# Kernel optimization log

Measured on AMD Instinct MI355X. Metric: run time of the kernel, lower is better.

## Reference

```python
import jax, jax.numpy as jnp
import numpy as np

N = 200000
D, H, W = 32, 480, 360   # sparse voxel grid (z, y, x)
CIN, COUT = 32, 64
BN_EPS = 1e-5


def _build_sparse_structure(seed=0):
    rng = np.random.default_rng(seed)
    lin = rng.choice(D * H * W, size=N, replace=False).astype(np.int64)
    d = lin // (H * W)
    h = (lin // W) % H
    w = lin % W
    lookup = np.full(D * H * W, -1, np.int32)
    lookup[lin] = np.arange(N, dtype=np.int32)

    def build_nbr(offsets):
        out = np.full((len(offsets), N), -1, np.int32)
        for k, (dd, dh, dw) in enumerate(offsets):
            nd, nh, nw = d + dd, h + dh, w + dw
            valid = (nd >= 0) & (nd < D) & (nh >= 0) & (nh < H) & (nw >= 0) & (nw < W)
            nl = (nd * H + nh) * W + nw
            out[k, valid] = lookup[nl[valid]]
        return out

    # conv1x3: kernel (1,3,3) -> offsets over (h, w)
    offs_a = [(0, dh, dw) for dh in (-1, 0, 1) for dw in (-1, 0, 1)]
    # conv3x1: kernel (3,1,3) -> offsets over (d, w)
    offs_b = [(dd, 0, dw) for dd in (-1, 0, 1) for dw in (-1, 0, 1)]
    return build_nbr(offs_a), build_nbr(offs_b)


def setup_inputs() -> dict:
    key = jax.random.key(0)
    ks = jax.random.split(key, 6)
    nbr_a, nbr_b = _build_sparse_structure()
    s = 0.05
    return {
        "feats": jax.random.normal(ks[0], (N, CIN), jnp.float32),
        "nbr_a": jnp.asarray(nbr_a),
        "nbr_b": jnp.asarray(nbr_b),
        "W1": jax.random.normal(ks[1], (9, CIN, COUT), jnp.float32) * s,
        "W1_2": jax.random.normal(ks[2], (9, COUT, COUT), jnp.float32) * s,
        "W2": jax.random.normal(ks[3], (9, CIN, COUT), jnp.float32) * s,
        "W3": jax.random.normal(ks[4], (9, COUT, COUT), jnp.float32) * s,
        "g0": jnp.ones((COUT,), jnp.float32), "b0": jnp.zeros((COUT,), jnp.float32),
        "g0_2": jnp.ones((COUT,), jnp.float32), "b0_2": jnp.zeros((COUT,), jnp.float32),
        "g1": jnp.ones((COUT,), jnp.float32), "b1": jnp.zeros((COUT,), jnp.float32),
        "g2": jnp.ones((COUT,), jnp.float32), "b2": jnp.zeros((COUT,), jnp.float32),
    }


def _subm_conv(x, nbr, Wk):
    # Submanifold sparse conv: gather neighbors per kernel offset, GEMM, sum.
    mask = (nbr >= 0)                                  # [K, N]
    g = x[jnp.clip(nbr, 0)] * mask[..., None]          # [K, N, Cin]
    return jnp.einsum('knc,kcd->nd', g, Wk)            # [N, Cout]


def _bn(x, g, b):
    # BatchNorm1d in training mode: biased batch stats over the voxel dim.
    m = jnp.mean(x, axis=0)
    v = jnp.var(x, axis=0)
    return g * (x - m) * jax.lax.rsqrt(v + BN_EPS) + b


def reference(feats, nbr_a, nbr_b, W1, W1_2, W2, W3,
              g0, b0, g0_2, b0_2, g1, b1, g2, b2):
    lrelu = lambda x: jax.nn.leaky_relu(x, 0.01)
    # shortcut branch: conv1x3 -> act -> bn -> conv3x1 -> bn
    sc = _subm_conv(feats, nbr_a, W1)
    sc = _bn(lrelu(sc), g0, b0)
    sc = _bn(_subm_conv(sc, nbr_b, W1_2), g0_2, b0_2)
    # main branch: conv3x1 -> act -> bn -> conv1x3 -> bn
    r = _subm_conv(feats, nbr_b, W2)
    r = _bn(lrelu(r), g1, b1)
    r = _bn(_subm_conv(r, nbr_a, W3), g2, b2)
    return r + sc
```

## Files before the change

### kernel.cpp

```cpp
#include <hip/hip_runtime.h>
#include <hip/hip_bf16.h>

#define NVOX 200000
#define CO 64

typedef short short8 __attribute__((ext_vector_type(8)));
typedef float f32x4 __attribute__((ext_vector_type(4)));

static __device__ __forceinline__ short f2bf(float f) {
    __hip_bfloat16 h = __float2bfloat16(f);
    return __builtin_bit_cast(short, h);
}

template<int CIN, bool IN_F32, bool LRELU, bool BIAS, bool OUT0_BF16, bool OUT1_BF16>
__global__ __launch_bounds__(320) void conv_mfma2(
    const void* __restrict__ xin0, const void* __restrict__ xin1,
    const int*  __restrict__ nbr0, const int* __restrict__ nbr1,
    const unsigned short* __restrict__ pack0, const unsigned short* __restrict__ pack1,
    const unsigned short* __restrict__ biasB0, const unsigned short* __restrict__ biasB1,
    void* __restrict__ out0, void* __restrict__ out1,
    float* __restrict__ ssum0, float* __restrict__ ssq0,
    float* __restrict__ ssum1, float* __restrict__ ssq1)
{
    constexpr int CHN = CIN / 32;
    const int br = blockIdx.y;
    const void* xin              = br ? xin1 : xin0;
    const int* nbr               = br ? nbr1 : nbr0;
    const unsigned short* bpack  = br ? pack1 : pack0;
    const unsigned short* biasB  = br ? biasB1 : biasB0;
    void* outp                   = br ? out1 : out0;
    float* s_sum                 = br ? ssum1 : ssum0;
    float* s_sq                  = br ? ssq1 : ssq0;
    const bool OUT_BF16          = br ? OUT1_BF16 : OUT0_BF16;

    const int lane = threadIdx.x & 63;
    const int wblk = threadIdx.x >> 6;
    const int wv   = blockIdx.x * 5 + wblk;
    const int gbase = wv * 32;
    const int g = lane >> 4, r16 = lane & 15;

    int iv[2][9];
    #pragma unroll
    for (int t = 0; t < 2; ++t)
        #pragma unroll
        for (int k = 0; k < 9; ++k)
            iv[t][k] = nbr[k * NVOX + gbase + t * 16 + r16];

    f32x4 acc[2][4];
    #pragma unroll
    for (int t = 0; t < 2; ++t)
        #pragma unroll
        for (int nt = 0; nt < 4; ++nt)
            acc[t][nt] = (f32x4){0.f, 0.f, 0.f, 0.f};

    #pragma unroll 3
    for (int k = 0; k < 9; ++k) {
        short8 bf[CHN][4];
        #pragma unroll
        for (int ch = 0; ch < CHN; ++ch)
            #pragma unroll
            for (int nt = 0; nt < 4; ++nt)
                bf[ch][nt] = *reinterpret_cast<const short8*>(
                    bpack + ((((size_t)k * CHN + ch) * 4 + nt) * 64 + lane) * 8);
        #pragma unroll
        for (int t = 0; t < 2; ++t) {
            const int ivk = iv[t][k];
            const int ivt = ivk < 0 ? 0 : ivk;
            #pragma unroll
            for (int ch = 0; ch < CHN; ++ch) {
                short8 av;
                if (IN_F32) {
                    const float* ap = (const float*)xin + (size_t)ivt * CIN + ch * 32 + g * 8;
                    float4 f0 = ((const float4*)ap)[0];
                    float4 f1 = ((const float4*)ap)[1];
                    av[0] = f2bf(f0.x); av[1] = f2bf(f0.y); av[2] = f2bf(f0.z); av[3] = f2bf(f0.w);
                    av[4] = f2bf(f1.x); av[5] = f2bf(f1.y); av[6] = f2bf(f1.z); av[7] = f2bf(f1.w);
                } else {
                    av = *reinterpret_cast<const short8*>(
                        (const unsigned short*)xin + (size_t)ivt * CIN + ch * 32 + g * 8);
                }
                if (ivk < 0) { short8 z = {0,0,0,0,0,0,0,0}; av = z; }
                #pragma unroll
                for (int nt = 0; nt < 4; ++nt)
                    acc[t][nt] = __builtin_amdgcn_mfma_f32_16x16x32_bf16(av, bf[ch][nt], acc[t][nt], 0, 0, 0);
            }
        }
    }

    if (BIAS) {
        short8 bb[4];
        #pragma unroll
        for (int nt = 0; nt < 4; ++nt)
            bb[nt] = *reinterpret_cast<const short8*>(biasB + ((size_t)nt * 64 + lane) * 8);
        #pragma unroll
        for (int t = 0; t < 2; ++t) {
            unsigned vmask = 0;
            #pragma unroll
            for (int k = 0; k < 9; ++k) vmask |= (iv[t][k] >= 0 ? 1u : 0u) << k;
            short8 vf;
            #pragma unroll
            for (int i = 0; i < 8; ++i) {
                int k9 = g * 8 + i;
                vf[i] = (k9 < 9 && ((vmask >> k9) & 1u)) ? (short)0x3F80 : (short)0;
            }
            #pragma unroll
            for (int nt = 0; nt < 4; ++nt)
                acc[t][nt] = __builtin_amdgcn_mfma_f32_16x16x32_bf16(vf, bb[nt], acc[t][nt], 0, 0, 0);
        }
    }

    float ss[4] = {0,0,0,0}, sq[4] = {0,0,0,0};
    #pragma unroll
    for (int t = 0; t < 2; ++t)
        #pragma unroll
        for (int nt = 0; nt < 4; ++nt)
            #pragma unroll
            for (int rr = 0; rr < 4; ++rr) {
                float val = acc[t][nt][rr];
                if (LRELU) val = val > 0.f ? val : 0.01f * val;
                ss[nt] += val; sq[nt] += val * val;
                const size_t o = (size_t)(gbase + t * 16 + g * 4 + rr) * CO + nt * 16 + r16;
                if (OUT_BF16) ((__hip_bfloat16*)outp)[o] = __float2bfloat16(val);
                else          ((float*)outp)[o] = val;
            }

    __shared__ float lsum[5][64];
    __shared__ float lsq[5][64];
    #pragma unroll
    for (int nt = 0; nt < 4; ++nt) {
        float a = ss[nt], b = sq[nt];
        a += __shfl_xor(a, 16); a += __shfl_xor(a, 32);
        b += __shfl_xor(b, 16); b += __shfl_xor(b, 32);
        if (lane < 16) { lsum[wblk][nt * 16 + r16] = a; lsq[wblk][nt * 16 + r16] = b; }
    }
    __syncthreads();
    if (threadIdx.x < 64) {
        float a = 0.f, b = 0.f;
        #pragma unroll
        for (int w = 0; w < 5; ++w) { a += lsum[w][threadIdx.x]; b += lsq[w][threadIdx.x]; }
        atomicAdd(s_sum + threadIdx.x, a);
        atomicAdd(s_sq  + threadIdx.x, b);
    }
}

__global__ void prepack_w32(const float* __restrict__ W1, const float* __restrict__ W2,
                            unsigned short* __restrict__ P1, unsigned short* __restrict__ P2)
{
    int s = blockIdx.x / 9, k = blockIdx.x % 9, l = threadIdx.x;
    const float* W = s ? W2 : W1;
    unsigned short* P = s ? P2 : P1;
    int g = l >> 4, r16 = l & 15;
    for (int nt = 0; nt < 4; ++nt)
        for (int i = 0; i < 8; ++i) {
            int c = g * 8 + i, j = nt * 16 + r16;
            P[(((size_t)k * 4 + nt) * 64 + l) * 8 + i] =
                (unsigned short)f2bf(W[((size_t)k * 32 + c) * 64 + j]);
        }
}

__global__ void bn_fin(const float* sum0, const float* sq0, const float* g0, const float* b0, float* a0, float* c0,
                       const float* sum1, const float* sq1, const float* g1, const float* b1, float* a1, float* c1)
{
    int j = threadIdx.x;
    const float inv_n = 1.f / (float)NVOX;
    if (blockIdx.x == 0) {
        float m = sum0[j] * inv_n;
        float v = sq0[j] * inv_n - m * m;
        float a = g0[j] * rsqrtf(v + 1e-5f);
        a0[j] = a; c0[j] = b0[j] - m * a;
    } else {
        float m = sum1[j] * inv_n;
        float v = sq1[j] * inv_n - m * m;
        float a = g1[j] * rsqrtf(v + 1e-5f);
        a1[j] = a; c1[j] = b1[j] - m * a;
    }
}

__global__ void wtrans(const float* W0, const float* a0v, const float* c0v, unsigned short* P0, float* bias0,
                       const float* W1, const float* a1v, const float* c1v, unsigned short* P1, float* bias1)
{
    int s = blockIdx.x / 9, k = blockIdx.x % 9, l = threadIdx.x;
    const float* W  = s ? W1 : W0;
    const float* av = s ? a1v : a0v;
    const float* cv = s ? c1v : c0v;
    unsigned short* P = s ? P1 : P0;
    float* bias = s ? bias1 : bias0;
    int g = l >> 4, r16 = l & 15;
    for (int ch = 0; ch < 2; ++ch)
        for (int nt = 0; nt < 4; ++nt)
            for (int i = 0; i < 8; ++i) {
                int c = ch * 32 + g * 8 + i, j = nt * 16 + r16;
                P[((((size_t)k * 2 + ch) * 4 + nt) * 64 + l) * 8 + i] =
                    (unsigned short)f2bf(av[c] * W[((size_t)k * 64 + c) * 64 + j]);
            }
    float bs = 0.f;
    for (int c = 0; c < 64; ++c) bs += cv[c] * W[((size_t)k * 64 + c) * 64 + l];
    bias[k * 64 + l] = bs;
}

__global__ void wpack_bias(const float* bias0, unsigned short* B0,
                           const float* bias1, unsigned short* B1)
{
    int s = blockIdx.x, l = threadIdx.x;
    const float* bias = s ? bias1 : bias0;
    unsigned short* B = s ? B1 : B0;
    int g = l >> 4, r16 = l & 15;
    for (int nt = 0; nt < 4; ++nt)
        for (int i = 0; i < 8; ++i) {
            int k9 = g * 8 + i;
            B[((size_t)nt * 64 + l) * 8 + i] =
                k9 < 9 ? (unsigned short)f2bf(bias[k9 * 64 + nt * 16 + r16]) : (unsigned short)0;
        }
}

__global__ void final_k(float* __restrict__ out, const __hip_bfloat16* __restrict__ sc2,
                        const float* __restrict__ a2, const float* __restrict__ c2,
                        const float* __restrict__ a02, const float* __restrict__ c02)
{
    int i = blockIdx.x * blockDim.x + threadIdx.x;
    if (i >= NVOX * CO) return;
    int ch = i & 63;
    float r = out[i];
    float s = __bfloat162float(sc2[i]);
    out[i] = a2[ch] * r + c2[ch] + a02[ch] * s + c02[ch];
}

extern "C" void kernel_launch(void* const* d_in, const int* in_sizes, int n_in,
                              void* d_out, int out_size, void* d_ws, size_t ws_size,
                              hipStream_t stream)
{
    const float* feats = (const float*)d_in[0];
    const int*   nbr_a = (const int*)d_in[1];
    const int*   nbr_b = (const int*)d_in[2];
    const float* W1    = (const float*)d_in[3];
    const float* W1_2  = (const float*)d_in[4];
    const float* W2    = (const float*)d_in[5];
    const float* W3    = (const float*)d_in[6];
    const float* g0    = (const float*)d_in[7];
    const float* b0    = (const float*)d_in[8];
    const float* g0_2  = (const float*)d_in[9];
    const float* b0_2  = (const float*)d_in[10];
    const float* g1    = (const float*)d_in[11];
    const float* b1    = (const float*)d_in[12];
    const float* g2    = (const float*)d_in[13];
    const float* b2    = (const float*)d_in[14];

    char* ws = (char*)d_ws;
    size_t off = 0;
    auto alloc = [&](size_t bytes) { void* p = ws + off; off += (bytes + 255) & ~(size_t)255; return p; };
    __hip_bfloat16* sc1 = (__hip_bfloat16*)alloc((size_t)NVOX * CO * 2);
    __hip_bfloat16* r1  = (__hip_bfloat16*)alloc((size_t)NVOX * CO * 2);
    __hip_bfloat16* sc2 = (__hip_bfloat16*)alloc((size_t)NVOX * CO * 2);
    unsigned short* P1a = (unsigned short*)alloc((size_t)9 * 4 * 64 * 8 * 2);
    unsigned short* P1b = (unsigned short*)alloc((size_t)9 * 4 * 64 * 8 * 2);
    unsigned short* P2a = (unsigned short*)alloc((size_t)9 * 2 * 4 * 64 * 8 * 2);
    unsigned short* P2b = (unsigned short*)alloc((size_t)9 * 2 * 4 * 64 * 8 * 2);
    unsigned short* Bba = (unsigned short*)alloc((size_t)4 * 64 * 8 * 2);
    unsigned short* Bbb = (unsigned short*)alloc((size_t)4 * 64 * 8 * 2);
    float* bias_sc = (float*)alloc(9 * 64 * 4);
    float* bias_r  = (float*)alloc(9 * 64 * 4);
    float* stats   = (float*)alloc(8 * 64 * 4);
    float* sum1a = stats,       *sq1a = stats + 64;
    float* sum1b = stats + 128, *sq1b = stats + 192;
    float* sum2a = stats + 256, *sq2a = stats + 320;
    float* sum2b = stats + 384, *sq2b = stats + 448;
    float* bn = (float*)alloc(8 * 64 * 4);
    float* a0 = bn,        *c0 = bn + 64;
    float* a1 = bn + 128,  *c1 = bn + 192;
    float* a02 = bn + 256, *c02 = bn + 320;
    float* a2 = bn + 384,  *c2 = bn + 448;

    hipMemsetAsync(stats, 0, 8 * 64 * 4, stream);

    const dim3 cgrid(1250, 2);
    const dim3 cblk(320);

    prepack_w32<<<18, 64, 0, stream>>>(W1, W2, P1a, P1b);

    conv_mfma2<32, true, true, false, true, true><<<cgrid, cblk, 0, stream>>>(
        feats, feats, nbr_a, nbr_b, P1a, P1b, nullptr, nullptr,
        sc1, r1, sum1a, sq1a, sum1b, sq1b);
    bn_fin<<<2, 64, 0, stream>>>(sum1a, sq1a, g0, b0, a0, c0, sum1b, sq1b, g1, b1, a1, c1);
    wtrans<<<18, 64, 0, stream>>>(W1_2, a0, c0, P2a, bias_sc, W3, a1, c1, P2b, bias_r);
    wpack_bias<<<2, 64, 0, stream>>>(bias_sc, Bba, bias_r, Bbb);
    conv_mfma2<64, false, false, true, true, false><<<cgrid, cblk, 0, stream>>>(
        sc1, r1, nbr_b, nbr_a, P2a, P2b, Bba, Bbb,
        sc2, d_out, sum2a, sq2a, sum2b, sq2b);
    bn_fin<<<2, 64, 0, stream>>>(sum2a, sq2a, g0_2, b0_2, a02, c02, sum2b, sq2b, g2, b2, a2, c2);
    final_k<<<(NVOX * CO + 255) / 256, 256, 0, stream>>>((float*)d_out, sc2, a2, c2, a02, c02);
}
```

Before: 313.7 us.

## Pre-cast feats to bf16, replace stat atomics with partials, vectorize final pass

A separate kernel converts the fp32 input features to bf16 once, so the first conv gathers 16-byte bf16 rows instead of 32-byte fp32 rows and converting them per neighbour. The BN statistic atomics are replaced by per-block partial sums that a dedicated reduce-and-finalize kernel folds, which also removes the memset. The k-loop is fully unrolled with launch bounds asking for 4 blocks per CU, and the final elementwise kernel handles 8 elements per thread. The extra cast pass adds a full read and write of feats, and the bf16 copy reuses the sc2 buffer.

```diff
diff --git a/kernel.cpp b/kernel.cpp
--- a/kernel.cpp
+++ b/kernel.cpp
@@ -11,26 +11,26 @@
     __hip_bfloat16 h = __float2bfloat16(f);
     return __builtin_bit_cast(short, h);
 }
-
-template<int CIN, bool IN_F32, bool LRELU, bool BIAS, bool OUT0_BF16, bool OUT1_BF16>
-__global__ __launch_bounds__(320) void conv_mfma2(
-    const void* __restrict__ xin0, const void* __restrict__ xin1,
+static __device__ __forceinline__ float bfu(unsigned short u) {
+    union { unsigned int i; float f; } x; x.i = ((unsigned int)u) << 16; return x.f;
+}
+
+template<int CIN, bool LRELU, bool BIAS, bool OUT0_BF16, bool OUT1_BF16>
+__global__ __launch_bounds__(320, 4) void conv_mfma2(
+    const unsigned short* __restrict__ xin0, const unsigned short* __restrict__ xin1,
     const int*  __restrict__ nbr0, const int* __restrict__ nbr1,
     const unsigned short* __restrict__ pack0, const unsigned short* __restrict__ pack1,
     const unsigned short* __restrict__ biasB0, const unsigned short* __restrict__ biasB1,
     void* __restrict__ out0, void* __restrict__ out1,
-    float* __restrict__ ssum0, float* __restrict__ ssq0,
-    float* __restrict__ ssum1, float* __restrict__ ssq1)
+    float* __restrict__ parts)
 {
     constexpr int CHN = CIN / 32;
     const int br = blockIdx.y;
-    const void* xin              = br ? xin1 : xin0;
+    const unsigned short* xin    = br ? xin1 : xin0;
     const int* nbr               = br ? nbr1 : nbr0;
     const unsigned short* bpack  = br ? pack1 : pack0;
     const unsigned short* biasB  = br ? biasB1 : biasB0;
     void* outp                   = br ? out1 : out0;
-    float* s_sum                 = br ? ssum1 : ssum0;
-    float* s_sq                  = br ? ssq1 : ssq0;
     const bool OUT_BF16          = br ? OUT1_BF16 : OUT0_BF16;
 
     const int lane = threadIdx.x & 63;
@@ -53,7 +53,7 @@
         for (int nt = 0; nt < 4; ++nt)
             acc[t][nt] = (f32x4){0.f, 0.f, 0.f, 0.f};
 
-    #pragma unroll 3
+    #pragma unroll
     for (int k = 0; k < 9; ++k) {
         short8 bf[CHN][4];
         #pragma unroll
@@ -68,17 +68,8 @@
             const int ivt = ivk < 0 ? 0 : ivk;
             #pragma unroll
             for (int ch = 0; ch < CHN; ++ch) {
-                short8 av;
-                if (IN_F32) {
-                    const float* ap = (const float*)xin + (size_t)ivt * CIN + ch * 32 + g * 8;
-                    float4 f0 = ((const float4*)ap)[0];
-                    float4 f1 = ((const float4*)ap)[1];
-                    av[0] = f2bf(f0.x); av[1] = f2bf(f0.y); av[2] = f2bf(f0.z); av[3] = f2bf(f0.w);
-                    av[4] = f2bf(f1.x); av[5] = f2bf(f1.y); av[6] = f2bf(f1.z); av[7] = f2bf(f1.w);
-                } else {
-                    av = *reinterpret_cast<const short8*>(
-                        (const unsigned short*)xin + (size_t)ivt * CIN + ch * 32 + g * 8);
-                }
+                short8 av = *reinterpret_cast<const short8*>(
+                    xin + (size_t)ivt * CIN + ch * 32 + g * 8);
                 if (ivk < 0) { short8 z = {0,0,0,0,0,0,0,0}; av = z; }
                 #pragma unroll
                 for (int nt = 0; nt < 4; ++nt)
@@ -138,9 +129,22 @@
         float a = 0.f, b = 0.f;
         #pragma unroll
         for (int w = 0; w < 5; ++w) { a += lsum[w][threadIdx.x]; b += lsq[w][threadIdx.x]; }
-        atomicAdd(s_sum + threadIdx.x, a);
-        atomicAdd(s_sq  + threadIdx.x, b);
-    }
+        float* dst = parts + ((size_t)blockIdx.y * gridDim.x + blockIdx.x) * 128;
+        dst[threadIdx.x] = a;
+        dst[64 + threadIdx.x] = b;
+    }
+}
+
+__global__ __launch_bounds__(256) void cast_feats(const float* __restrict__ in,
+                                                  unsigned short* __restrict__ outp)
+{
+    const int i = (blockIdx.x * 256 + threadIdx.x) * 8;
+    float4 f0 = ((const float4*)(in + i))[0];
+    float4 f1 = ((const float4*)(in + i))[1];
+    short8 v;
+    v[0] = f2bf(f0.x); v[1] = f2bf(f0.y); v[2] = f2bf(f0.z); v[3] = f2bf(f0.w);
+    v[4] = f2bf(f1.x); v[5] = f2bf(f1.y); v[6] = f2bf(f1.z); v[7] = f2bf(f1.w);
+    *reinterpret_cast<short8*>(outp + i) = v;
 }
 
 __global__ void prepack_w32(const float* __restrict__ W1, const float* __restrict__ W2,
@@ -158,21 +162,33 @@
         }
 }
 
-__global__ void bn_fin(const float* sum0, const float* sq0, const float* g0, const float* b0, float* a0, float* c0,
-                       const float* sum1, const float* sq1, const float* g1, const float* b1, float* a1, float* c1)
-{
-    int j = threadIdx.x;
-    const float inv_n = 1.f / (float)NVOX;
-    if (blockIdx.x == 0) {
-        float m = sum0[j] * inv_n;
-        float v = sq0[j] * inv_n - m * m;
-        float a = g0[j] * rsqrtf(v + 1e-5f);
-        a0[j] = a; c0[j] = b0[j] - m * a;
-    } else {
-        float m = sum1[j] * inv_n;
-        float v = sq1[j] * inv_n - m * m;
-        float a = g1[j] * rsqrtf(v + 1e-5f);
-        a1[j] = a; c1[j] = b1[j] - m * a;
+__global__ __launch_bounds__(512) void bn_reduce_fin(
+    const float* __restrict__ parts,
+    const float* g_0, const float* b_0, float* a_0, float* c_0,
+    const float* g_1, const float* b_1, float* a_1, float* c_1)
+{
+    const int br = blockIdx.x;
+    const float* P = parts + (size_t)br * 1250 * 128;
+    const int tid = threadIdx.x;
+    const int col = tid & 127, seg = tid >> 7;
+    float s = 0.f;
+    for (int i = seg; i < 1250; i += 4) s += P[(size_t)i * 128 + col];
+    __shared__ float red[4][128];
+    red[seg][col] = s;
+    __syncthreads();
+    if (seg == 0) red[0][col] = red[0][col] + red[1][col] + red[2][col] + red[3][col];
+    __syncthreads();
+    if (tid < 64) {
+        const float inv_n = 1.f / (float)NVOX;
+        float m = red[0][tid] * inv_n;
+        float v = red[0][64 + tid] * inv_n - m * m;
+        const float* g = br ? g_1 : g_0;
+        const float* b = br ? b_1 : b_0;
+        float* a = br ? a_1 : a_0;
+        float* c = br ? c_1 : c_0;
+        float av = g[tid] * rsqrtf(v + 1e-5f);
+        a[tid] = av;
+        c[tid] = b[tid] - m * av;
     }
 }
 
@@ -213,16 +229,27 @@
         }
 }
 
-__global__ void final_k(float* __restrict__ out, const __hip_bfloat16* __restrict__ sc2,
-                        const float* __restrict__ a2, const float* __restrict__ c2,
-                        const float* __restrict__ a02, const float* __restrict__ c02)
-{
-    int i = blockIdx.x * blockDim.x + threadIdx.x;
-    if (i >= NVOX * CO) return;
-    int ch = i & 63;
-    float r = out[i];
-    float s = __bfloat162float(sc2[i]);
-    out[i] = a2[ch] * r + c2[ch] + a02[ch] * s + c02[ch];
+__global__ __launch_bounds__(256) void final_k8(
+    float* __restrict__ out, const __hip_bfloat16* __restrict__ sc2,
+    const float* __restrict__ a2, const float* __restrict__ c2,
+    const float* __restrict__ a02, const float* __restrict__ c02)
+{
+    const int i = (blockIdx.x * 256 + threadIdx.x) * 8;
+    const int ch0 = i & 63;
+    float4 r0 = ((const float4*)(out + i))[0];
+    float4 r1 = ((const float4*)(out + i))[1];
+    short8 s = *reinterpret_cast<const short8*>((const unsigned short*)sc2 + i);
+    float rr[8] = {r0.x, r0.y, r0.z, r0.w, r1.x, r1.y, r1.z, r1.w};
+    float res[8];
+    #pragma unroll
+    for (int j = 0; j < 8; ++j) {
+        int ch = ch0 + j;
+        res[j] = a2[ch] * rr[j] + c2[ch] + a02[ch] * bfu((unsigned short)s[j]) + c02[ch];
+    }
+    float4 o0 = {res[0], res[1], res[2], res[3]};
+    float4 o1 = {res[4], res[5], res[6], res[7]};
+    ((float4*)(out + i))[0] = o0;
+    ((float4*)(out + i))[1] = o1;
 }
 
 extern "C" void kernel_launch(void* const* d_in, const int* in_sizes, int n_in,
@@ -251,6 +278,7 @@
     __hip_bfloat16* sc1 = (__hip_bfloat16*)alloc((size_t)NVOX * CO * 2);
     __hip_bfloat16* r1  = (__hip_bfloat16*)alloc((size_t)NVOX * CO * 2);
     __hip_bfloat16* sc2 = (__hip_bfloat16*)alloc((size_t)NVOX * CO * 2);
+    unsigned short* featsbf = (unsigned short*)sc2;
     unsigned short* P1a = (unsigned short*)alloc((size_t)9 * 4 * 64 * 8 * 2);
     unsigned short* P1b = (unsigned short*)alloc((size_t)9 * 4 * 64 * 8 * 2);
     unsigned short* P2a = (unsigned short*)alloc((size_t)9 * 2 * 4 * 64 * 8 * 2);
@@ -259,33 +287,29 @@
     unsigned short* Bbb = (unsigned short*)alloc((size_t)4 * 64 * 8 * 2);
     float* bias_sc = (float*)alloc(9 * 64 * 4);
     float* bias_r  = (float*)alloc(9 * 64 * 4);
-    float* stats   = (float*)alloc(8 * 64 * 4);
-    float* sum1a = stats,       *sq1a = stats + 64;
-    float* sum1b = stats + 128, *sq1b = stats + 192;
-    float* sum2a = stats + 256, *sq2a = stats + 320;
-    float* sum2b = stats + 384, *sq2b = stats + 448;
+    float* parts1  = (float*)alloc((size_t)2 * 1250 * 128 * 4);
+    float* parts2  = (float*)alloc((size_t)2 * 1250 * 128 * 4);
     float* bn = (float*)alloc(8 * 64 * 4);
     float* a0 = bn,        *c0 = bn + 64;
     float* a1 = bn + 128,  *c1 = bn + 192;
     float* a02 = bn + 256, *c02 = bn + 320;
     float* a2 = bn + 384,  *c2 = bn + 448;
 
-    hipMemsetAsync(stats, 0, 8 * 64 * 4, stream);
-
     const dim3 cgrid(1250, 2);
     const dim3 cblk(320);
 
+    cast_feats<<<3125, 256, 0, stream>>>(feats, featsbf);
     prepack_w32<<<18, 64, 0, stream>>>(W1, W2, P1a, P1b);
 
-    conv_mfma2<32, true, true, false, true, true><<<cgrid, cblk, 0, stream>>>(
-        feats, feats, nbr_a, nbr_b, P1a, P1b, nullptr, nullptr,
-        sc1, r1, sum1a, sq1a, sum1b, sq1b);
-    bn_fin<<<2, 64, 0, stream>>>(sum1a, sq1a, g0, b0, a0, c0, sum1b, sq1b, g1, b1, a1, c1);
+    conv_mfma2<32, true, false, true, true><<<cgrid, cblk, 0, stream>>>(
+        featsbf, featsbf, nbr_a, nbr_b, P1a, P1b, nullptr, nullptr,
+        sc1, r1, parts1);
+    bn_reduce_fin<<<2, 512, 0, stream>>>(parts1, g0, b0, a0, c0, g1, b1, a1, c1);
     wtrans<<<18, 64, 0, stream>>>(W1_2, a0, c0, P2a, bias_sc, W3, a1, c1, P2b, bias_r);
     wpack_bias<<<2, 64, 0, stream>>>(bias_sc, Bba, bias_r, Bbb);
-    conv_mfma2<64, false, false, true, true, false><<<cgrid, cblk, 0, stream>>>(
-        sc1, r1, nbr_b, nbr_a, P2a, P2b, Bba, Bbb,
-        sc2, d_out, sum2a, sq2a, sum2b, sq2b);
-    bn_fin<<<2, 64, 0, stream>>>(sum2a, sq2a, g0_2, b0_2, a02, c02, sum2b, sq2b, g2, b2, a2, c2);
-    final_k<<<(NVOX * CO + 255) / 256, 256, 0, stream>>>((float*)d_out, sc2, a2, c2, a02, c02);
-}
+    conv_mfma2<64, false, true, true, false><<<cgrid, cblk, 0, stream>>>(
+        (const unsigned short*)sc1, (const unsigned short*)r1, nbr_b, nbr_a,
+        P2a, P2b, Bba, Bbb, sc2, d_out, parts2);
+    bn_reduce_fin<<<2, 512, 0, stream>>>(parts2, g0_2, b0_2, a02, c02, g2, b2, a2, c2);
+    final_k8<<<6250, 256, 0, stream>>>((float*)d_out, sc2, a2, c2, a02, c02);
+}
```

Result: slower. 410.3 us (+30.8%).
